# Performance work log

Hardware: AMD Instinct MI355X
Metric: run time of the kernel (lower is better)

The kernel has to match this reference:

```python
import jax, jax.numpy as jnp
import numpy as np

DN = ('NCDHW', 'DHWIO', 'NCDHW')


def _w(key, cin, cout):
    # kernel_size=3 in 3D, Minkowski-style fan-in scaling, no bias
    scale = 1.0 / np.sqrt(cin * 27)
    return jax.random.normal(key, (3, 3, 3, cin, cout), dtype=jnp.float32) * scale


def setup_inputs() -> dict:
    key = jax.random.key(0)
    ks = jax.random.split(key, 7)
    x = jax.random.normal(ks[0], (1, 1024, 4, 4, 4), dtype=jnp.float32)
    chans = [(1024, 512), (512, 256), (256, 128), (128, 64), (64, 32), (32, 1)]
    ws = {f'w{i+1}': _w(ks[i + 1], ci, co) for i, (ci, co) in enumerate(chans)}
    return {'x': x, **ws}


def _ct(x, w, stride):
    # conv-transpose, kernel 3, SAME padding: stride 2 doubles resolution,
    # stride 1 preserves it (dense analog of Minkowski generative transpose conv)
    return jax.lax.conv_transpose(x, w, strides=(stride, stride, stride),
                                  padding='SAME', dimension_numbers=DN)


def reference(x, w1, w2, w3, w4, w5, w6):
    h = jax.nn.relu(_ct(x, w1, 2))   # 1024 -> 512, 4^3 -> 8^3
    h = jax.nn.relu(_ct(h, w2, 1))   # 512 -> 256
    h = jax.nn.relu(_ct(h, w3, 2))   # 256 -> 128, 8^3 -> 16^3
    h = jax.nn.relu(_ct(h, w4, 1))   # 128 -> 64
    h = jax.nn.relu(_ct(h, w5, 2))   # 64 -> 32, 16^3 -> 32^3
    return _ct(h, w6, 1)             # 32 -> 1, no final ReLU
```

## Files before the change

kernel.cpp:

```cpp
#include <hip/hip_runtime.h>

typedef _Float16 half8 __attribute__((ext_vector_type(8)));
typedef _Float16 half4v __attribute__((ext_vector_type(4)));
typedef float floatx4 __attribute__((ext_vector_type(4)));


__global__ __launch_bounds__(256) void pad_x_k(const float* __restrict__ X,
                                               _Float16* __restrict__ P) {
  int idx = blockIdx.x * 256 + threadIdx.x;
  if (idx >= 125 * 1024) return;
  int c = idx & 1023;
  int r = idx >> 10;
  int px = r % 5, py = (r / 5) % 5, pz = r / 25;
  float v = 0.f;
  if (px >= 1 && py >= 1 && pz >= 1)
    v = X[c * 64 + (pz - 1) * 16 + (py - 1) * 4 + (px - 1)];
  P[idx] = (_Float16)v;
}

__device__ __forceinline__ half8 cvt_relu8(const float4& f0, const float4& f1) {
  half8 h;
  h[0] = (_Float16)fmaxf(f0.x, 0.f);
  h[1] = (_Float16)fmaxf(f0.y, 0.f);
  h[2] = (_Float16)fmaxf(f0.z, 0.f);
  h[3] = (_Float16)fmaxf(f0.w, 0.f);
  h[4] = (_Float16)fmaxf(f1.x, 0.f);
  h[5] = (_Float16)fmaxf(f1.y, 0.f);
  h[6] = (_Float16)fmaxf(f1.z, 0.f);
  h[7] = (_Float16)fmaxf(f1.w, 0.f);
  return h;
}

template <int CICHUNK, int CIN, int COUT, int NTILE, int TZ, int SOUTU,
          int SMODE, int TAPG, int IN_MODE, int STORE_MODE>
__global__ __launch_bounds__(256) void conv_mfma_k(
    const void* __restrict__ Pin, const float* __restrict__ W,
    void* __restrict__ Optr) {
  constexpr int M = TZ * 16;
  constexpr bool S2 = (SMODE != 0);
  constexpr int MTZ = SOUTU / TZ;
  constexpr int MTXY = SOUTU / 4;
  constexpr int MT3 = MTZ * MTXY * MTXY;
  constexpr int KB = 32;
  constexpr int KP = 40;
  constexpr int KBI = CICHUNK / KB;
  constexpr int NCI = CIN / CICHUNK;
  constexpr int S = S2 ? 2 * SOUTU : SOUTU;
  constexpr int WM = (M == 128) ? 4 : 2;
  constexpr int NSUB = (WM == 4) ? (NTILE / 16) : (NTILE / 32);
  constexpr int BJ = KB * NTILE / 256;

  __shared__ __align__(16) _Float16 As[M][KP];
  __shared__ __align__(16) _Float16 Bs[NTILE][KP];

  int bx = blockIdx.x;
  int cls = 0, tap0 = 0, cig = blockIdx.z;
  int p_toz = 0, p_toy = 0, p_tox = 0, p_wtap = 0;
  if (SMODE == 0) {
    const int tg = cig / NCI;
    cig -= tg * NCI;
    tap0 = tg * TAPG;
  } else if (SMODE == 1) {
    const int p = bx / MT3;
    bx -= p * MT3;
    cls = (p >= 8) + (p >= 12) + (p >= 16) + (p >= 18) + (p >= 22) +
          (p >= 24) + (p >= 26);
    const int pf = cls == 0 ? 0 : cls == 1 ? 8 : cls == 2 ? 12
                 : cls == 3 ? 16 : cls == 4 ? 18 : cls == 5 ? 22
                 : cls == 6 ? 24 : 26;
    const int tl = p - pf;
    const int lz = (cls >> 2) & 1, ly = (cls >> 1) & 1, lx = cls & 1;
    const int shx = lx ? 0 : 1, shy = ly ? 0 : 1;
    const int iz = tl >> (shx + shy);
    const int rem = tl & ((1 << (shx + shy)) - 1);
    const int iy = rem >> shx;
    const int ix = rem & ((1 << shx) - 1);
    p_toz = lz ? 1 : iz;
    p_toy = ly ? 1 : iy;
    p_tox = lx ? 1 : ix;
    const int wz = lz ? 1 : 2 * iz, wy = ly ? 1 : 2 * iy,
              wx = lx ? 1 : 2 * ix;
    p_wtap = (wz * 3 + wy) * 3 + wx;
  } else {
    cls = bx / MT3;
    bx -= cls * MT3;
  }
  const int clz = (cls >> 2) & 1, cly = (cls >> 1) & 1, clx = cls & 1;

  const int u0z = (bx / (MTXY * MTXY)) * TZ;
  const int u0y = ((bx / MTXY) % MTXY) * 4;
  const int u0x = (bx % MTXY) * 4;
  const int n_base = blockIdx.y * NTILE;

  const int t = threadIdx.x;
  const int lane = t & 63;
  const int wave = t >> 6;

  const int skq = t & 3;
  const int sp = t >> 2;
  const int spx = sp & 3, spy = (sp >> 2) & 3, spz = sp >> 4;
  const int nB = t & (NTILE - 1);
  const int k0B = (t / NTILE) * BJ;
  const int m0w = (WM == 4) ? wave * 32 : (wave >> 1) * 32;
  const int n0w = (WM == 4) ? 0 : (wave & 1) * 32;
  const int fr = lane & 15;
  const int fq = lane >> 4;

  const int cz = S2 ? (clz ? 1 : 2) : 3;
  const int cy = S2 ? (cly ? 1 : 2) : 3;
  const int cx = S2 ? (clx ? 1 : 2) : 3;
  const int shx2 = clx ? 0 : 1, shy2 = cly ? 0 : 1;

  int NIT;
  if (SMODE == 0) NIT = TAPG * KBI;
  else if (SMODE == 1) NIT = KBI;
  else NIT = cz * cy * cx * KBI;

  floatx4 acc[2][NSUB];
#pragma unroll
  for (int i = 0; i < 2; i++)
#pragma unroll
    for (int s = 0; s < NSUB; s++) acc[i][s] = {0.f, 0.f, 0.f, 0.f};

  half8 rA0 = {}, rA1 = {}, nA0 = {}, nA1 = {};
  float rB[BJ] = {}, nBv[BJ] = {};

  auto load_it = [&](int it, half8& A0, half8& A1, float* BW) {
    int tap, kb;
    if (SMODE == 1) { tap = 0; kb = it; }
    else if (KBI == 1) { tap = it; kb = 0; }
    else { tap = it / KBI; kb = it - tap * KBI; }
    int toz, toy, tox, wtap;
    if (SMODE == 1) {
      toz = p_toz; toy = p_toy; tox = p_tox; wtap = p_wtap;
    } else if (SMODE == 0) {
      const int tt = tap0 + tap;
      const int iz = tt / 9;
      const int rem = tt - iz * 9;
      const int iy = rem / 3;
      const int ix = rem - iy * 3;
      toz = iz; toy = iy; tox = ix;
      wtap = tt;
    } else {
      const int iz = tap >> (shx2 + shy2);
      const int rem = tap & ((1 << (shx2 + shy2)) - 1);
      const int iy = rem >> shx2;
      const int ix = rem & ((1 << shx2) - 1);
      toz = clz ? 1 : iz; toy = cly ? 1 : iy; tox = clx ? 1 : ix;
      const int wz = clz ? 1 : 2 * iz, wy = cly ? 1 : 2 * iy,
                wx = clx ? 1 : 2 * ix;
      wtap = (wz * 3 + wy) * 3 + wx;
    }
    const int kof0 = cig * CICHUNK + kb * KB;
    if (IN_MODE == 0) {
      constexpr int PS = SOUTU + 1;
      const _Float16* Pp = (const _Float16*)Pin;
      const size_t pb =
          ((size_t)(((u0z + toz + spz) * PS + (u0y + toy + spy)) * PS +
                    (u0x + tox + spx))) * CIN + kof0 + skq * 8;
      A0 = *(const half8*)(Pp + pb);
      if (M == 128)
        A1 = *(const half8*)(Pp + pb + (size_t)4 * PS * PS * CIN);
    } else {
      const float* Ip = (const float*)Pin;
      const int izc = u0z + toz + spz - 1;
      const int iyc = u0y + toy + spy - 1;
      const int ixc = u0x + tox + spx - 1;
      const bool okyx = ((unsigned)iyc < (unsigned)SOUTU) &
                        ((unsigned)ixc < (unsigned)SOUTU);
      const float* src =
          Ip + ((size_t)((izc * SOUTU + iyc) * SOUTU + ixc)) * CIN + kof0 +
          skq * 8;
      float4 f0 = make_float4(0.f, 0.f, 0.f, 0.f);
      float4 f1 = make_float4(0.f, 0.f, 0.f, 0.f);
      if (okyx && ((unsigned)izc < (unsigned)SOUTU)) {
        f0 = *(const float4*)src;
        f1 = *(const float4*)(src + 4);
      }
      A0 = cvt_relu8(f0, f1);
      if (M == 128) {
        float4 g0 = make_float4(0.f, 0.f, 0.f, 0.f);
        float4 g1 = make_float4(0.f, 0.f, 0.f, 0.f);
        if (okyx && ((unsigned)(izc + 4) < (unsigned)SOUTU)) {
          const float* s2p = src + (size_t)4 * SOUTU * SOUTU * CIN;
          g0 = *(const float4*)s2p;
          g1 = *(const float4*)(s2p + 4);
        }
        A1 = cvt_relu8(g0, g1);
      }
    }
    const float* wb =
        W + ((size_t)wtap * CIN + kof0 + k0B) * COUT + n_base + nB;
#pragma unroll
    for (int j = 0; j < BJ; j++) BW[j] = wb[(size_t)j * COUT];
  };

  load_it(0, rA0, rA1, rB);

  for (int it = 0; it < NIT; ++it) {
    *(half8*)&As[sp][skq * 8] = rA0;
    if (M == 128) *(half8*)&As[sp + 64][skq * 8] = rA1;
    if (BJ == 8) {
      half8 hb;
#pragma unroll
      for (int j = 0; j < 8; j++) hb[j] = (_Float16)rB[j];
      *(half8*)&Bs[nB][k0B] = hb;
    } else {
      half4v hb;
#pragma unroll
      for (int j = 0; j < 4; j++) hb[j] = (_Float16)rB[j];
      *(half4v*)&Bs[nB][k0B] = hb;
    }
    __syncthreads();
    if (it + 1 < NIT) load_it(it + 1, nA0, nA1, nBv);
    half8 a0 = *(const half8*)&As[m0w + fr][fq * 8];
    half8 a1 = *(const half8*)&As[m0w + 16 + fr][fq * 8];
#pragma unroll
    for (int s = 0; s < NSUB; s++) {
      half8 b = *(const half8*)&Bs[n0w + s * 16 + fr][fq * 8];
      acc[0][s] = __builtin_amdgcn_mfma_f32_16x16x32_f16(a0, b, acc[0][s], 0, 0, 0);
      acc[1][s] = __builtin_amdgcn_mfma_f32_16x16x32_f16(a1, b, acc[1][s], 0, 0, 0);
    }
    __syncthreads();
    rA0 = nA0;
    rA1 = nA1;
#pragma unroll
    for (int j = 0; j < BJ; j++) rB[j] = nBv[j];
  }

#pragma unroll
  for (int i = 0; i < 2; i++) {
#pragma unroll
    for (int r = 0; r < 4; r++) {
      const int m = m0w + i * 16 + fq * 4 + r;
      const int mz = m >> 4, my = (m >> 2) & 3, mx = m & 3;
      int oz, oy, ox;
      if (S2) {
        oz = 2 * (u0z + mz) + clz;
        oy = 2 * (u0y + my) + cly;
        ox = 2 * (u0x + mx) + clx;
      } else {
        oz = u0z + mz;
        oy = u0y + my;
        ox = u0x + mx;
      }
      if (STORE_MODE == 2) {
        _Float16* o = (_Float16*)Optr +
            ((size_t)(((oz + 1) * (S + 2) + (oy + 1)) * (S + 2) + (ox + 1))) *
                COUT + n_base + n0w;
#pragma unroll
        for (int s = 0; s < NSUB; s++)
          o[s * 16 + fr] = (_Float16)fmaxf(acc[i][s][r], 0.f);
      } else {
        float* o = (float*)Optr +
            ((size_t)((oz * S + oy) * S + ox)) * COUT + n_base + n0w;
#pragma unroll
        for (int s = 0; s < NSUB; s++) atomicAdd(o + s * 16 + fr, acc[i][s][r]);
      }
    }
  }
}

__global__ __launch_bounds__(256) void conv6_k(const _Float16* __restrict__ P,
                                               const float* __restrict__ W6,
                                               float* __restrict__ O) {
  __shared__ __align__(16) float w[864];
  for (int i = threadIdx.x; i < 864; i += 256) w[i] = W6[i];
  __syncthreads();
  int idx = blockIdx.x * 256 + threadIdx.x;
  int x = idx & 31, y = (idx >> 5) & 31, z = idx >> 10;
  float a = 0.f;
  for (int dz = 0; dz < 3; dz++)
    for (int dy = 0; dy < 3; dy++)
      for (int dx = 0; dx < 3; dx++) {
        const _Float16* p =
            P + (size_t)(((z + dz) * 34 + (y + dy)) * 34 + (x + dx)) * 32;
        const float* ww = &w[((dz * 3 + dy) * 3 + dx) * 32];
#pragma unroll
        for (int c = 0; c < 32; c += 8) {
          half8 pv = *(const half8*)&p[c];
#pragma unroll
          for (int u = 0; u < 8; u++) a += (float)pv[u] * ww[c + u];
        }
      }
  O[idx] = a;
}

extern "C" void kernel_launch(void* const* d_in, const int* in_sizes, int n_in,
                              void* d_out, int out_size, void* d_ws,
                              size_t ws_size, hipStream_t stream) {
  const float* x  = (const float*)d_in[0];
  const float* w1 = (const float*)d_in[1];
  const float* w2 = (const float*)d_in[2];
  const float* w3 = (const float*)d_in[3];
  const float* w4 = (const float*)d_in[4];
  const float* w5 = (const float*)d_in[5];
  const float* w6 = (const float*)d_in[6];
  float* out = (float*)d_out;

  float* O1 = (float*)d_ws;
  float* O2 = O1 + 262144;
  float* O3 = O2 + 131072;
  float* O4 = O3 + 524288;
  _Float16* P6 = (_Float16*)(O4 + 262144);
  _Float16* P1 = P6 + 1257728;

  hipMemsetAsync(d_ws, 0,
                 1179648 * sizeof(float) + 1257728 * sizeof(_Float16), stream);

  pad_x_k<<<500, 256, 0, stream>>>(x, P1);
  conv_mfma_k<256, 1024, 512, 64, 4, 4, 1, 0, 0, 1>
      <<<dim3(27, 8, 4), 256, 0, stream>>>(P1, w1, O1);
  conv_mfma_k<64, 512, 256, 64, 8, 8, 0, 9, 1, 1>
      <<<dim3(4, 4, 24), 256, 0, stream>>>(O1, w2, O2);
  conv_mfma_k<128, 256, 128, 64, 8, 8, 1, 0, 1, 1>
      <<<dim3(108, 2, 2), 256, 0, stream>>>(O2, w3, O3);
  conv_mfma_k<32, 128, 64, 64, 8, 16, 0, 9, 1, 1>
      <<<dim3(32, 1, 12), 256, 0, stream>>>(O3, w4, O4);
  conv_mfma_k<64, 64, 32, 32, 8, 16, 2, 0, 1, 2>
      <<<dim3(256, 1, 1), 256, 0, stream>>>(O4, w5, P6);
  conv6_k<<<128, 256, 0, stream>>>(P6, w6, out);

  (void)in_sizes; (void)n_in; (void)out_size; (void)ws_size;
}
```

Measured before the change: 221.7 us.

## Replace atomicAdd split-K accumulation with partial buffers plus reduction kernels

```diff
diff --git a/kernel.cpp b/kernel.cpp
--- a/kernel.cpp
+++ b/kernel.cpp
@@ -18,23 +18,54 @@
   P[idx] = (_Float16)v;
 }
 
-__device__ __forceinline__ half8 cvt_relu8(const float4& f0, const float4& f1) {
-  half8 h;
-  h[0] = (_Float16)fmaxf(f0.x, 0.f);
-  h[1] = (_Float16)fmaxf(f0.y, 0.f);
-  h[2] = (_Float16)fmaxf(f0.z, 0.f);
-  h[3] = (_Float16)fmaxf(f0.w, 0.f);
-  h[4] = (_Float16)fmaxf(f1.x, 0.f);
-  h[5] = (_Float16)fmaxf(f1.y, 0.f);
-  h[6] = (_Float16)fmaxf(f1.z, 0.f);
-  h[7] = (_Float16)fmaxf(f1.w, 0.f);
-  return h;
+template <int POS, int COUT, int S2IN, int NSPL, int PS>
+__global__ __launch_bounds__(256) void red_k(const float* __restrict__ Pp,
+                                             _Float16* __restrict__ P) {
+  constexpr int C4 = COUT / 4;
+  constexpr size_t U3 =
+      S2IN ? (size_t)(POS / 2) * (POS / 2) * (POS / 2) : (size_t)POS * POS * POS;
+  int idx = blockIdx.x * 256 + threadIdx.x;
+  if (idx >= PS * PS * PS * C4) return;
+  const int co = (idx % C4) * 4;
+  const int r = idx / C4;
+  const int px = r % PS, py = (r / PS) % PS, pz = r / (PS * PS);
+  const int ix = px - 1, iy = py - 1, iz = pz - 1;
+  float4 s = make_float4(0.f, 0.f, 0.f, 0.f);
+  if ((unsigned)ix < (unsigned)POS && (unsigned)iy < (unsigned)POS &&
+      (unsigned)iz < (unsigned)POS) {
+    int j0, j1;
+    size_t upos;
+    if (S2IN) {
+      const int pf[8] = {0, 8, 12, 16, 18, 22, 24, 26};
+      const int tc[8] = {8, 4, 4, 2, 4, 2, 2, 1};
+      const int cls = ((iz & 1) << 2) | ((iy & 1) << 1) | (ix & 1);
+      j0 = pf[cls] * NSPL;
+      j1 = j0 + tc[cls] * NSPL;
+      constexpr int U = POS / 2;
+      upos = ((size_t)(iz >> 1) * U + (iy >> 1)) * U + (ix >> 1);
+    } else {
+      j0 = 0;
+      j1 = NSPL;
+      upos = ((size_t)iz * POS + iy) * POS + ix;
+    }
+    const float* base = Pp + upos * COUT + co;
+    for (int j = j0; j < j1; j++) {
+      float4 v = *(const float4*)(base + (size_t)j * U3 * COUT);
+      s.x += v.x; s.y += v.y; s.z += v.z; s.w += v.w;
+    }
+  }
+  half4v h;
+  h[0] = (_Float16)fmaxf(s.x, 0.f);
+  h[1] = (_Float16)fmaxf(s.y, 0.f);
+  h[2] = (_Float16)fmaxf(s.z, 0.f);
+  h[3] = (_Float16)fmaxf(s.w, 0.f);
+  *(half4v*)(P + (size_t)idx * 4) = h;
 }
 
 template <int CICHUNK, int CIN, int COUT, int NTILE, int TZ, int SOUTU,
-          int SMODE, int TAPG, int IN_MODE, int STORE_MODE>
+          int PS, int SMODE, int TAPG, int STORE_MODE>
 __global__ __launch_bounds__(256) void conv_mfma_k(
-    const void* __restrict__ Pin, const float* __restrict__ W,
+    const _Float16* __restrict__ P, const float* __restrict__ W,
     void* __restrict__ Optr) {
   constexpr int M = TZ * 16;
   constexpr bool S2 = (SMODE != 0);
@@ -49,20 +80,23 @@
   constexpr int WM = (M == 128) ? 4 : 2;
   constexpr int NSUB = (WM == 4) ? (NTILE / 16) : (NTILE / 32);
   constexpr int BJ = KB * NTILE / 256;
+  constexpr size_t U3 = (size_t)SOUTU * SOUTU * SOUTU;
 
   __shared__ __align__(16) _Float16 As[M][KP];
   __shared__ __align__(16) _Float16 Bs[NTILE][KP];
 
   int bx = blockIdx.x;
-  int cls = 0, tap0 = 0, cig = blockIdx.z;
+  int cls = 0, tap0 = 0, cig = blockIdx.z, jspl = 0;
   int p_toz = 0, p_toy = 0, p_tox = 0, p_wtap = 0;
   if (SMODE == 0) {
     const int tg = cig / NCI;
     cig -= tg * NCI;
     tap0 = tg * TAPG;
+    jspl = blockIdx.z;
   } else if (SMODE == 1) {
     const int p = bx / MT3;
     bx -= p * MT3;
+    jspl = p * NCI + cig;
     cls = (p >= 8) + (p >= 12) + (p >= 16) + (p >= 18) + (p >= 22) +
           (p >= 24) + (p >= 26);
     const int pf = cls == 0 ? 0 : cls == 1 ? 8 : cls == 2 ? 12
@@ -152,43 +186,12 @@
       wtap = (wz * 3 + wy) * 3 + wx;
     }
     const int kof0 = cig * CICHUNK + kb * KB;
-    if (IN_MODE == 0) {
-      constexpr int PS = SOUTU + 1;
-      const _Float16* Pp = (const _Float16*)Pin;
-      const size_t pb =
-          ((size_t)(((u0z + toz + spz) * PS + (u0y + toy + spy)) * PS +
-                    (u0x + tox + spx))) * CIN + kof0 + skq * 8;
-      A0 = *(const half8*)(Pp + pb);
-      if (M == 128)
-        A1 = *(const half8*)(Pp + pb + (size_t)4 * PS * PS * CIN);
-    } else {
-      const float* Ip = (const float*)Pin;
-      const int izc = u0z + toz + spz - 1;
-      const int iyc = u0y + toy + spy - 1;
-      const int ixc = u0x + tox + spx - 1;
-      const bool okyx = ((unsigned)iyc < (unsigned)SOUTU) &
-                        ((unsigned)ixc < (unsigned)SOUTU);
-      const float* src =
-          Ip + ((size_t)((izc * SOUTU + iyc) * SOUTU + ixc)) * CIN + kof0 +
-          skq * 8;
-      float4 f0 = make_float4(0.f, 0.f, 0.f, 0.f);
-      float4 f1 = make_float4(0.f, 0.f, 0.f, 0.f);
-      if (okyx && ((unsigned)izc < (unsigned)SOUTU)) {
-        f0 = *(const float4*)src;
-        f1 = *(const float4*)(src + 4);
-      }
-      A0 = cvt_relu8(f0, f1);
-      if (M == 128) {
-        float4 g0 = make_float4(0.f, 0.f, 0.f, 0.f);
-        float4 g1 = make_float4(0.f, 0.f, 0.f, 0.f);
-        if (okyx && ((unsigned)(izc + 4) < (unsigned)SOUTU)) {
-          const float* s2p = src + (size_t)4 * SOUTU * SOUTU * CIN;
-          g0 = *(const float4*)s2p;
-          g1 = *(const float4*)(s2p + 4);
-        }
-        A1 = cvt_relu8(g0, g1);
-      }
-    }
+    const size_t pb =
+        ((size_t)(((u0z + toz + spz) * PS + (u0y + toy + spy)) * PS +
+                  (u0x + tox + spx))) * CIN + kof0 + skq * 8;
+    A0 = *(const half8*)(P + pb);
+    if (M == 128)
+      A1 = *(const half8*)(P + pb + (size_t)4 * PS * PS * CIN);
     const float* wb =
         W + ((size_t)wtap * CIN + kof0 + k0B) * COUT + n_base + nB;
 #pragma unroll
@@ -234,17 +237,10 @@
     for (int r = 0; r < 4; r++) {
       const int m = m0w + i * 16 + fq * 4 + r;
       const int mz = m >> 4, my = (m >> 2) & 3, mx = m & 3;
-      int oz, oy, ox;
-      if (S2) {
-        oz = 2 * (u0z + mz) + clz;
-        oy = 2 * (u0y + my) + cly;
-        ox = 2 * (u0x + mx) + clx;
-      } else {
-        oz = u0z + mz;
-        oy = u0y + my;
-        ox = u0x + mx;
-      }
       if (STORE_MODE == 2) {
+        const int oz = 2 * (u0z + mz) + clz;
+        const int oy = 2 * (u0y + my) + cly;
+        const int ox = 2 * (u0x + mx) + clx;
         _Float16* o = (_Float16*)Optr +
             ((size_t)(((oz + 1) * (S + 2) + (oy + 1)) * (S + 2) + (ox + 1))) *
                 COUT + n_base + n0w;
@@ -252,10 +248,12 @@
         for (int s = 0; s < NSUB; s++)
           o[s * 16 + fr] = (_Float16)fmaxf(acc[i][s][r], 0.f);
       } else {
-        float* o = (float*)Optr +
-            ((size_t)((oz * S + oy) * S + ox)) * COUT + n_base + n0w;
-#pragma unroll
-        for (int s = 0; s < NSUB; s++) atomicAdd(o + s * 16 + fr, acc[i][s][r]);
+        const size_t pos =
+            ((size_t)((u0z + mz) * SOUTU + (u0y + my))) * SOUTU + (u0x + mx);
+        float* o = (float*)Optr + ((size_t)jspl * U3 + pos) * COUT + n_base +
+                   n0w;
+#pragma unroll
+        for (int s = 0; s < NSUB; s++) o[s * 16 + fr] = acc[i][s][r];
       }
     }
   }
@@ -298,27 +296,34 @@
   const float* w6 = (const float*)d_in[6];
   float* out = (float*)d_out;
 
-  float* O1 = (float*)d_ws;
-  float* O2 = O1 + 262144;
-  float* O3 = O2 + 131072;
-  float* O4 = O3 + 524288;
-  _Float16* P6 = (_Float16*)(O4 + 262144);
-  _Float16* P1 = P6 + 1257728;
-
-  hipMemsetAsync(d_ws, 0,
-                 1179648 * sizeof(float) + 1257728 * sizeof(_Float16), stream);
+  float* Q1 = (float*)d_ws;
+  float* Q2 = Q1 + 3538944;
+  float* Q3 = Q2 + 3145728;
+  float* Q4 = Q3 + 3538944;
+  _Float16* P1 = (_Float16*)(Q4 + 3145728);
+  _Float16* P2 = P1 + 128000;
+  _Float16* P3 = P2 + 512000;
+  _Float16* P4 = P3 + 186624;
+  _Float16* P5 = P4 + 746496;
+  _Float16* P6 = P5 + 314432;
+
+  hipMemsetAsync(P6, 0, 1257728 * sizeof(_Float16), stream);
 
   pad_x_k<<<500, 256, 0, stream>>>(x, P1);
-  conv_mfma_k<256, 1024, 512, 64, 4, 4, 1, 0, 0, 1>
-      <<<dim3(27, 8, 4), 256, 0, stream>>>(P1, w1, O1);
-  conv_mfma_k<64, 512, 256, 64, 8, 8, 0, 9, 1, 1>
-      <<<dim3(4, 4, 24), 256, 0, stream>>>(O1, w2, O2);
-  conv_mfma_k<128, 256, 128, 64, 8, 8, 1, 0, 1, 1>
-      <<<dim3(108, 2, 2), 256, 0, stream>>>(O2, w3, O3);
-  conv_mfma_k<32, 128, 64, 64, 8, 16, 0, 9, 1, 1>
-      <<<dim3(32, 1, 12), 256, 0, stream>>>(O3, w4, O4);
-  conv_mfma_k<64, 64, 32, 32, 8, 16, 2, 0, 1, 2>
-      <<<dim3(256, 1, 1), 256, 0, stream>>>(O4, w5, P6);
+  conv_mfma_k<256, 1024, 512, 64, 4, 4, 5, 1, 0, 3>
+      <<<dim3(27, 8, 4), 256, 0, stream>>>(P1, w1, Q1);
+  red_k<8, 512, 1, 4, 10><<<500, 256, 0, stream>>>(Q1, P2);
+  conv_mfma_k<64, 512, 256, 64, 8, 8, 10, 0, 9, 3>
+      <<<dim3(4, 4, 24), 256, 0, stream>>>(P2, w2, Q2);
+  red_k<8, 256, 0, 24, 9><<<183, 256, 0, stream>>>(Q2, P3);
+  conv_mfma_k<128, 256, 128, 64, 8, 8, 9, 1, 0, 3>
+      <<<dim3(108, 2, 2), 256, 0, stream>>>(P3, w3, Q3);
+  red_k<16, 128, 1, 2, 18><<<729, 256, 0, stream>>>(Q3, P4);
+  conv_mfma_k<32, 128, 64, 64, 8, 16, 18, 0, 9, 3>
+      <<<dim3(32, 1, 12), 256, 0, stream>>>(P4, w4, Q4);
+  red_k<16, 64, 0, 12, 17><<<308, 256, 0, stream>>>(Q4, P5);
+  conv_mfma_k<64, 64, 32, 32, 8, 16, 17, 2, 0, 2>
+      <<<dim3(256, 1, 1), 256, 0, stream>>>(P5, w5, P6);
   conv6_k<<<128, 256, 0, stream>>>(P6, w6, out);
 
   (void)in_sizes; (void)n_in; (void)out_size; (void)ws_size;
```

After: 208.5 us. 1.06x faster.
